# Kernel optimization log

Hardware: AMD Instinct MI355X
Metric: run time of the kernel (lower is better)

## Reference

```python
import jax, jax.numpy as jnp
import numpy as np
import math

MODEL_DIM = 256
NUM_HEADS = 8
HEAD_DIM = MODEL_DIM // NUM_HEADS
DEMAND_DIM = 3
H, W = 128, 256
N_COLLAB = 4


def conv1x1(x, w, b):
    # x: [B, Cin, H, W], w: [Cout, Cin], b: [Cout]
    return jnp.einsum('oi,bihw->bohw', w, x) + b[None, :, None, None]


def setup_inputs() -> dict:
    key = jax.random.key(0)
    ks = jax.random.split(key, 16)
    s = 0.02
    hid = MODEL_DIM // 2
    inp = {
        'ego_features': jax.random.normal(ks[0], (1, MODEL_DIM, H, W), jnp.float32),
        'ego_demand': jax.random.uniform(ks[1], (1, DEMAND_DIM, H, W), jnp.float32),
        'collaborator_features': jax.random.normal(ks[2], (N_COLLAB, MODEL_DIM, H, W), jnp.float32),
        'w_d1': jax.random.normal(ks[3], (hid, DEMAND_DIM), jnp.float32) * s,
        'b_d1': jnp.zeros((hid,), jnp.float32),
        'w_d2': jax.random.normal(ks[4], (MODEL_DIM, hid), jnp.float32) * s,
        'b_d2': jnp.zeros((MODEL_DIM,), jnp.float32),
        'wq': jax.random.normal(ks[5], (MODEL_DIM, MODEL_DIM), jnp.float32) * s,
        'bq': jnp.zeros((MODEL_DIM,), jnp.float32),
        'wk': jax.random.normal(ks[6], (MODEL_DIM, MODEL_DIM), jnp.float32) * s,
        'bk': jnp.zeros((MODEL_DIM,), jnp.float32),
        'wv': jax.random.normal(ks[7], (MODEL_DIM, MODEL_DIM), jnp.float32) * s,
        'bv': jnp.zeros((MODEL_DIM,), jnp.float32),
        'wo': jax.random.normal(ks[8], (MODEL_DIM, MODEL_DIM), jnp.float32) * s,
        'bo': jnp.zeros((MODEL_DIM,), jnp.float32),
        'pos_emb': jnp.zeros((1, MODEL_DIM, H, W), jnp.float32),
    }
    return inp


def reference(ego_features, ego_demand, collaborator_features,
              w_d1, b_d1, w_d2, b_d2, wq, bq, wk, bk, wv, bv, wo, bo, pos_emb):
    # demand encoder: 1x1 conv -> relu -> 1x1 conv
    enc = conv1x1(jax.nn.relu(conv1x1(ego_demand, w_d1, b_d1)), w_d2, b_d2)
    query_state = ego_features + enc + pos_emb  # [1, C, H, W]

    q = conv1x1(query_state, wq, bq).reshape(NUM_HEADS, HEAD_DIM, H, W)        # [M, d, H, W]
    k = conv1x1(collaborator_features, wk, bk).reshape(N_COLLAB, NUM_HEADS, HEAD_DIM, H, W)
    v = conv1x1(collaborator_features, wv, bv).reshape(N_COLLAB, NUM_HEADS, HEAD_DIM, H, W)

    scale = math.sqrt(HEAD_DIM)
    # per-pixel dot product over head_dim -> scores [N, M, H, W]
    scores = jnp.einsum('mdhw,nmdhw->nmhw', q, k) / scale
    attn = jax.nn.softmax(scores, axis=0)  # softmax over collaborators
    # weighted sum over collaborators -> [M, d, H, W]
    out = jnp.einsum('nmhw,nmdhw->mdhw', attn, v).reshape(1, MODEL_DIM, H, W)
    return conv1x1(out, wo, bo)  # [1, C, H, W]
```

## Files before the change

### kernel.cpp

```cpp
#include <hip/hip_runtime.h>
#include <stdint.h>

typedef __attribute__((ext_vector_type(8))) short short8;
typedef __attribute__((ext_vector_type(4))) float f32x4;

constexpr int C   = 256;
constexpr int HID = 128;
constexpr int P   = 32768;
constexpr int BN  = 64;
constexpr int XLD = 280;
constexpr int HLD = 136;

constexpr unsigned OFF_WQ  = 0;
constexpr unsigned OFF_WK  = 65536;
constexpr unsigned OFF_WV  = 131072;
constexpr unsigned OFF_WO  = 196608;
constexpr unsigned OFF_WD2 = 262144;
constexpr unsigned W_TOTAL = 294912;

__device__ __forceinline__ unsigned f2b(float x) {
    unsigned u = __float_as_uint(x);
    return (u + 0x7FFFu + ((u >> 16) & 1u)) >> 16;
}
__device__ __forceinline__ float b2f(unsigned u) {
    return __uint_as_float(u << 16);
}

__global__ void cvt_weights(const float* __restrict__ wq, const float* __restrict__ wk,
                            const float* __restrict__ wv, const float* __restrict__ wo,
                            const float* __restrict__ wd2, unsigned short* __restrict__ dst) {
    unsigned i = blockIdx.x * 256 + threadIdx.x;
    if (i >= W_TOTAL) return;
    float v;
    if (i < OFF_WK)       v = wq[i];
    else if (i < OFF_WV)  v = wk[i - OFF_WK];
    else if (i < OFF_WO)  v = wv[i - OFF_WV];
    else if (i < OFF_WD2) v = wo[i - OFF_WO];
    else                  v = wd2[i - OFF_WD2];
    dst[i] = (unsigned short)f2b(v);
}


template <int K, int LD, int MI, bool SWZ>
__device__ __forceinline__ void gemmW(const unsigned short* __restrict__ W,
                                      const unsigned short* __restrict__ B,
                                      int row0, int a, int q, f32x4 (*acc)[4]) {
#pragma unroll 2
    for (int ks = 0; ks < K / 32; ++ks) {
        const int kb = ks * 32 + q * 8;
        short8 af[MI], bf[4];
#pragma unroll
        for (int mi = 0; mi < MI; ++mi)
            af[mi] = *reinterpret_cast<const short8*>(W + (size_t)(row0 + mi * 16 + a) * K + kb);
#pragma unroll
        for (int ni = 0; ni < 4; ++ni) {
            const int col = SWZ ? (kb ^ (((2 * ni + (a >> 3)) & 7) << 3)) : kb;
            bf[ni] = *reinterpret_cast<const short8*>(B + (ni * 16 + a) * LD + col);
        }
#pragma unroll
        for (int mi = 0; mi < MI; ++mi)
#pragma unroll
            for (int ni = 0; ni < 4; ++ni)
                acc[mi][ni] = __builtin_amdgcn_mfma_f32_16x16x32_bf16(af[mi], bf[ni], acc[mi][ni], 0, 0, 0);
    }
}

__device__ __forceinline__ void stage_ego(const float* __restrict__ s0,
                                          const float* __restrict__ s1,
                                          int t, int pix0, unsigned short* X) {
    const int cg = t >> 4;
    const int pb = 4 * (t & 15);
    const int swz = (((t & 15) >> 1) & 7) << 3;
#pragma unroll
    for (int k = 0; k < 4; ++k) {
        const int c = 2 * cg + 64 * k;
        const int cs = c ^ swz;
        float4 ra = *reinterpret_cast<const float4*>(s0 + (size_t)c * P + pix0 + pb);
        float4 rb = *reinterpret_cast<const float4*>(s0 + (size_t)(c + 1) * P + pix0 + pb);
        float4 ta = *reinterpret_cast<const float4*>(s1 + (size_t)c * P + pix0 + pb);
        float4 tb = *reinterpret_cast<const float4*>(s1 + (size_t)(c + 1) * P + pix0 + pb);
        ra.x += ta.x; ra.y += ta.y; ra.z += ta.z; ra.w += ta.w;
        rb.x += tb.x; rb.y += tb.y; rb.z += tb.z; rb.w += tb.w;
        const float va[4] = {ra.x, ra.y, ra.z, ra.w};
        const float vb[4] = {rb.x, rb.y, rb.z, rb.w};
#pragma unroll
        for (int pi = 0; pi < 4; ++pi) {
            unsigned pk = f2b(va[pi]) | (f2b(vb[pi]) << 16);
            *reinterpret_cast<unsigned*>(X + (pb + pi) * XLD + cs) = pk;
        }
    }
}

__device__ __forceinline__ void issue_half(const float* __restrict__ src, int pix0,
                                           int t, int k0, float4* s4) {
    const int cg = t >> 4;
    const int pb = 4 * (t & 15);
#pragma unroll
    for (int kk = 0; kk < 2; ++kk) {
        const int c = 2 * cg + 64 * (k0 + kk);
        s4[2 * kk]     = *reinterpret_cast<const float4*>(src + (size_t)c * P + pix0 + pb);
        s4[2 * kk + 1] = *reinterpret_cast<const float4*>(src + (size_t)(c + 1) * P + pix0 + pb);
    }
}

__device__ __forceinline__ void convert_half(unsigned short* X, int t, int k0,
                                             const float4* s4) {
    const int cg = t >> 4;
    const int pb = 4 * (t & 15);
    const int swz = (((t & 15) >> 1) & 7) << 3;
#pragma unroll
    for (int kk = 0; kk < 2; ++kk) {
        const int cs = (2 * cg + 64 * (k0 + kk)) ^ swz;
        const float4 ra = s4[2 * kk], rb = s4[2 * kk + 1];
        const float va[4] = {ra.x, ra.y, ra.z, ra.w};
        const float vb[4] = {rb.x, rb.y, rb.z, rb.w};
#pragma unroll
        for (int pi = 0; pi < 4; ++pi) {
            unsigned pk = f2b(va[pi]) | (f2b(vb[pi]) << 16);
            *reinterpret_cast<unsigned*>(X + (pb + pi) * XLD + cs) = pk;
        }
    }
}

__global__ __launch_bounds__(512, 2) void dca_mfma(
    const float* __restrict__ ego, const float* __restrict__ dem,
    const float* __restrict__ col,
    const float* __restrict__ w_d1, const float* __restrict__ b_d1,
    const float* __restrict__ b_d2, const float* __restrict__ bq,
    const float* __restrict__ bk, const float* __restrict__ bv,
    const float* __restrict__ bo, const float* __restrict__ pos,
    const unsigned short* __restrict__ wbf, float* __restrict__ out)
{
    __shared__ __align__(16) unsigned short xbuf[2 * BN * XLD];
    unsigned short* const x0 = xbuf;
    unsigned short* const x1 = xbuf + BN * XLD;

    const int t = threadIdx.x;
    const int w = t >> 6;
    const int l = t & 63;
    const int a = l & 15;
    const int q = l >> 4;
    const int row0 = w * 32;
    const int pix0 = blockIdx.x * BN;

    stage_ego(ego, pos, t, pix0, x0);

    {
        const int hid0 = 2 * l;
        const float w10 = w_d1[hid0 * 3 + 0], w11 = w_d1[hid0 * 3 + 1], w12 = w_d1[hid0 * 3 + 2];
        const float w20 = w_d1[hid0 * 3 + 3], w21 = w_d1[hid0 * 3 + 4], w22 = w_d1[hid0 * 3 + 5];
        const float bb0 = b_d1[hid0], bb1 = b_d1[hid0 + 1];
#pragma unroll
        for (int k = 0; k < 8; ++k) {
            const int p = w + 8 * k;
            float d0 = dem[pix0 + p];
            float d1 = dem[P + pix0 + p];
            float d2v = dem[2 * P + pix0 + p];
            float h0 = fmaxf(bb0 + w10 * d0 + w11 * d1 + w12 * d2v, 0.0f);
            float h1v = fmaxf(bb1 + w20 * d0 + w21 * d1 + w22 * d2v, 0.0f);
            *reinterpret_cast<unsigned*>(x1 + p * HLD + hid0) = f2b(h0) | (f2b(h1v) << 16);
        }
    }
    __syncthreads();

    f32x4 vacc[2][4];

#pragma unroll
    for (int mi = 0; mi < 2; ++mi) {
        f32x4 bb = *reinterpret_cast<const f32x4*>(b_d2 + row0 + mi * 16 + q * 4);
#pragma unroll
        for (int ni = 0; ni < 4; ++ni) vacc[mi][ni] = bb;
    }
    gemmW<HID, HLD, 2, false>(wbf + OFF_WD2, x1, row0, a, q, vacc);
#pragma unroll
    for (int mi = 0; mi < 2; ++mi) {
        const int cb = row0 + mi * 16 + q * 4;
#pragma unroll
        for (int ni = 0; ni < 4; ++ni) {
            const int row = ni * 16 + a;
            const int cs = cb ^ (((2 * ni + (a >> 3)) & 7) << 3);
            unsigned* cell = reinterpret_cast<unsigned*>(x0 + row * XLD + cs);
            unsigned e0 = cell[0], e1 = cell[1];
            float o0 = vacc[mi][ni][0] + b2f(e0 & 0xFFFFu);
            float o1 = vacc[mi][ni][1] + b2f(e0 >> 16);
            float o2 = vacc[mi][ni][2] + b2f(e1 & 0xFFFFu);
            float o3 = vacc[mi][ni][3] + b2f(e1 >> 16);
            cell[0] = f2b(o0) | (f2b(o1) << 16);
            cell[1] = f2b(o2) | (f2b(o3) << 16);
        }
    }
    __syncthreads();

    float4 sA[4], sB[4];
    issue_half(col, pix0, t, 0, sA);

#pragma unroll
    for (int mi = 0; mi < 2; ++mi) {
        f32x4 bb = *reinterpret_cast<const f32x4*>(bq + row0 + mi * 16 + q * 4);
#pragma unroll
        for (int ni = 0; ni < 4; ++ni) vacc[mi][ni] = bb;
    }
    gemmW<C, XLD, 2, true>(wbf + OFF_WQ, x0, row0, a, q, vacc);
    unsigned qpk[2][4][2];
#pragma unroll
    for (int mi = 0; mi < 2; ++mi)
#pragma unroll
        for (int ni = 0; ni < 4; ++ni) {
            qpk[mi][ni][0] = f2b(vacc[mi][ni][0]) | (f2b(vacc[mi][ni][1]) << 16);
            qpk[mi][ni][1] = f2b(vacc[mi][ni][2]) | (f2b(vacc[mi][ni][3]) << 16);
        }

    convert_half(x1, t, 0, sA);
    issue_half(col, pix0, t, 2, sB);
    convert_half(x1, t, 2, sB);
    issue_half(col + (size_t)C * P, pix0, t, 0, sA);
    __syncthreads();

    float lrun[4];
#pragma unroll
    for (int ni = 0; ni < 4; ++ni) lrun[ni] = 0.0f;
    {
        const f32x4 z = {0.0f, 0.0f, 0.0f, 0.0f};
#pragma unroll
        for (int mi = 0; mi < 2; ++mi)
#pragma unroll
            for (int ni = 0; ni < 4; ++ni) vacc[mi][ni] = z;
    }
#pragma unroll 1
    for (int n = 0; n < 4; ++n) {
        unsigned short* const rbuf = (n & 1) ? x0 : x1;
        unsigned short* const wbuf = (n & 1) ? x1 : x0;
        float s[4];
#pragma unroll
        for (int ni = 0; ni < 4; ++ni) s[ni] = 0.0f;
        {
            f32x4 kacc[2][4];
#pragma unroll
            for (int mi = 0; mi < 2; ++mi) {
                f32x4 bb = *reinterpret_cast<const f32x4*>(bk + row0 + mi * 16 + q * 4);
#pragma unroll
                for (int ni = 0; ni < 4; ++ni) kacc[mi][ni] = bb;
            }
            gemmW<C, XLD, 2, true>(wbf + OFF_WK, rbuf, row0, a, q, kacc);
#pragma unroll
            for (int mi = 0; mi < 2; ++mi)
#pragma unroll
                for (int ni = 0; ni < 4; ++ni) {
                    const unsigned u0 = qpk[mi][ni][0], u1 = qpk[mi][ni][1];
                    float ps = s[ni];
                    ps += b2f(u0 & 0xFFFFu) * kacc[mi][ni][0];
                    ps += b2f(u0 >> 16)     * kacc[mi][ni][1];
                    ps += b2f(u1 & 0xFFFFu) * kacc[mi][ni][2];
                    ps += b2f(u1 >> 16)     * kacc[mi][ni][3];
                    s[ni] = ps;
                }
        }
        if (n < 3) {
            convert_half(wbuf, t, 0, sA);
            issue_half(col + (size_t)(n + 1) * C * P, pix0, t, 2, sB);
        }
        float pp[4];
#pragma unroll
        for (int ni = 0; ni < 4; ++ni) {
            float ps = s[ni];
            ps += __shfl_xor(ps, 16);
            ps += __shfl_xor(ps, 32);
            pp[ni] = __expf(ps * 0.17677669529663687f);
            lrun[ni] += pp[ni];
        }
#pragma unroll
        for (int ni = 0; ni < 4; ++ni) {
            const float ip = 1.0f / pp[ni];
#pragma unroll
            for (int mi = 0; mi < 2; ++mi) vacc[mi][ni] *= ip;
        }
        gemmW<C, XLD, 2, true>(wbf + OFF_WV, rbuf, row0, a, q, vacc);
#pragma unroll
        for (int ni = 0; ni < 4; ++ni) {
#pragma unroll
            for (int mi = 0; mi < 2; ++mi) vacc[mi][ni] *= pp[ni];
        }
        if (n < 3) convert_half(wbuf, t, 2, sB);
        if (n < 2) issue_half(col + (size_t)(n + 2) * C * P, pix0, t, 0, sA);
        __syncthreads();
    }
#pragma unroll
    for (int ni = 0; ni < 4; ++ni) {
        float inv = 1.0f / lrun[ni];
#pragma unroll
        for (int mi = 0; mi < 2; ++mi) vacc[mi][ni] *= inv;
    }
#pragma unroll
    for (int mi = 0; mi < 2; ++mi) {
        f32x4 bb = *reinterpret_cast<const f32x4*>(bv + row0 + mi * 16 + q * 4);
#pragma unroll
        for (int ni = 0; ni < 4; ++ni) vacc[mi][ni] += bb;
    }

#pragma unroll
    for (int mi = 0; mi < 2; ++mi) {
        const int cb = row0 + mi * 16 + q * 4;
#pragma unroll
        for (int ni = 0; ni < 4; ++ni) {
            const int row = ni * 16 + a;
            const int cs = cb ^ (((2 * ni + (a >> 3)) & 7) << 3);
            unsigned* cell = reinterpret_cast<unsigned*>(x0 + row * XLD + cs);
            cell[0] = f2b(vacc[mi][ni][0]) | (f2b(vacc[mi][ni][1]) << 16);
            cell[1] = f2b(vacc[mi][ni][2]) | (f2b(vacc[mi][ni][3]) << 16);
        }
    }
    __syncthreads();
#pragma unroll
    for (int mi = 0; mi < 2; ++mi) {
        f32x4 bb = *reinterpret_cast<const f32x4*>(bo + row0 + mi * 16 + q * 4);
#pragma unroll
        for (int ni = 0; ni < 4; ++ni) vacc[mi][ni] = bb;
    }
    gemmW<C, XLD, 2, true>(wbf + OFF_WO, x0, row0, a, q, vacc);
#pragma unroll
    for (int mi = 0; mi < 2; ++mi) {
        const int cb = row0 + mi * 16 + q * 4;
#pragma unroll
        for (int ni = 0; ni < 4; ++ni) {
            const int pix = pix0 + ni * 16 + a;
#pragma unroll
            for (int r = 0; r < 4; ++r)
                out[(size_t)(cb + r) * P + pix] = vacc[mi][ni][r];
        }
    }
}

extern "C" void kernel_launch(void* const* d_in, const int* in_sizes, int n_in,
                              void* d_out, int out_size, void* d_ws, size_t ws_size,
                              hipStream_t stream) {
    const float* ego  = (const float*)d_in[0];
    const float* dem  = (const float*)d_in[1];
    const float* col  = (const float*)d_in[2];
    const float* w_d1 = (const float*)d_in[3];
    const float* b_d1 = (const float*)d_in[4];
    const float* w_d2 = (const float*)d_in[5];
    const float* b_d2 = (const float*)d_in[6];
    const float* wq   = (const float*)d_in[7];
    const float* bq   = (const float*)d_in[8];
    const float* wk   = (const float*)d_in[9];
    const float* bk   = (const float*)d_in[10];
    const float* wv   = (const float*)d_in[11];
    const float* bv   = (const float*)d_in[12];
    const float* wo   = (const float*)d_in[13];
    const float* bo   = (const float*)d_in[14];
    const float* pos  = (const float*)d_in[15];
    float* out = (float*)d_out;
    unsigned short* wbf = (unsigned short*)d_ws;

    hipLaunchKernelGGL(cvt_weights, dim3((W_TOTAL + 255) / 256), dim3(256), 0, stream,
                       wq, wk, wv, wo, w_d2, wbf);
    hipLaunchKernelGGL(dca_mfma, dim3(P / BN), dim3(512), 0, stream,
                       ego, dem, col, w_d1, b_d1, b_d2, bq, bk, bv, bo, pos, wbf, out);
}
```

Baseline: 334.8 us.

## Use four LDS buffers to stage collaborator tiles with fewer barriers

Moves from two double-buffered LDS tiles to four, so all collaborator feature tiles are staged in whole-tile chunks (8 float4 loads per thread) instead of halves. This cuts the per-iteration __syncthreads, leaving one barrier mid-loop and one after it, and starts the first collaborator load earlier, before the demand GEMM. LDS use per block doubles to about 140KB, which likely cuts occupancy from two blocks per CU to one despite launch_bounds(512,2). Doubling the in-flight prefetch registers also adds register pressure.

```diff
diff --git a/kernel.cpp b/kernel.cpp
--- a/kernel.cpp
+++ b/kernel.cpp
@@ -91,27 +91,26 @@
     }
 }
 
-__device__ __forceinline__ void issue_half(const float* __restrict__ src, int pix0,
-                                           int t, int k0, float4* s4) {
+__device__ __forceinline__ void issue_tile(const float* __restrict__ src, int pix0,
+                                           int t, float4* s4) {
     const int cg = t >> 4;
     const int pb = 4 * (t & 15);
 #pragma unroll
-    for (int kk = 0; kk < 2; ++kk) {
-        const int c = 2 * cg + 64 * (k0 + kk);
-        s4[2 * kk]     = *reinterpret_cast<const float4*>(src + (size_t)c * P + pix0 + pb);
-        s4[2 * kk + 1] = *reinterpret_cast<const float4*>(src + (size_t)(c + 1) * P + pix0 + pb);
-    }
-}
-
-__device__ __forceinline__ void convert_half(unsigned short* X, int t, int k0,
-                                             const float4* s4) {
+    for (int k = 0; k < 4; ++k) {
+        const int c = 2 * cg + 64 * k;
+        s4[2 * k]     = *reinterpret_cast<const float4*>(src + (size_t)c * P + pix0 + pb);
+        s4[2 * k + 1] = *reinterpret_cast<const float4*>(src + (size_t)(c + 1) * P + pix0 + pb);
+    }
+}
+
+__device__ __forceinline__ void convert_tile(unsigned short* X, int t, const float4* s4) {
     const int cg = t >> 4;
     const int pb = 4 * (t & 15);
     const int swz = (((t & 15) >> 1) & 7) << 3;
 #pragma unroll
-    for (int kk = 0; kk < 2; ++kk) {
-        const int cs = (2 * cg + 64 * (k0 + kk)) ^ swz;
-        const float4 ra = s4[2 * kk], rb = s4[2 * kk + 1];
+    for (int k = 0; k < 4; ++k) {
+        const int cs = (2 * cg + 64 * k) ^ swz;
+        const float4 ra = s4[2 * k], rb = s4[2 * k + 1];
         const float va[4] = {ra.x, ra.y, ra.z, ra.w};
         const float vb[4] = {rb.x, rb.y, rb.z, rb.w};
 #pragma unroll
@@ -131,9 +130,11 @@
     const float* __restrict__ bo, const float* __restrict__ pos,
     const unsigned short* __restrict__ wbf, float* __restrict__ out)
 {
-    __shared__ __align__(16) unsigned short xbuf[2 * BN * XLD];
-    unsigned short* const x0 = xbuf;
-    unsigned short* const x1 = xbuf + BN * XLD;
+    __shared__ __align__(16) unsigned short xbuf[4 * BN * XLD];
+    unsigned short* const bufA = xbuf;
+    unsigned short* const bufB = xbuf + 1 * BN * XLD;
+    unsigned short* const bufC = xbuf + 2 * BN * XLD;
+    unsigned short* const bufD = xbuf + 3 * BN * XLD;
 
     const int t = threadIdx.x;
     const int w = t >> 6;
@@ -143,7 +144,7 @@
     const int row0 = w * 32;
     const int pix0 = blockIdx.x * BN;
 
-    stage_ego(ego, pos, t, pix0, x0);
+    stage_ego(ego, pos, t, pix0, bufA);
 
     {
         const int hid0 = 2 * l;
@@ -158,10 +159,13 @@
             float d2v = dem[2 * P + pix0 + p];
             float h0 = fmaxf(bb0 + w10 * d0 + w11 * d1 + w12 * d2v, 0.0f);
             float h1v = fmaxf(bb1 + w20 * d0 + w21 * d1 + w22 * d2v, 0.0f);
-            *reinterpret_cast<unsigned*>(x1 + p * HLD + hid0) = f2b(h0) | (f2b(h1v) << 16);
-        }
-    }
-    __syncthreads();
+            *reinterpret_cast<unsigned*>(bufD + p * HLD + hid0) = f2b(h0) | (f2b(h1v) << 16);
+        }
+    }
+    __syncthreads();
+
+    float4 sA[8];
+    issue_tile(col, pix0, t, sA);
 
     f32x4 vacc[2][4];
 
@@ -171,7 +175,7 @@
 #pragma unroll
         for (int ni = 0; ni < 4; ++ni) vacc[mi][ni] = bb;
     }
-    gemmW<HID, HLD, 2, false>(wbf + OFF_WD2, x1, row0, a, q, vacc);
+    gemmW<HID, HLD, 2, false>(wbf + OFF_WD2, bufD, row0, a, q, vacc);
 #pragma unroll
     for (int mi = 0; mi < 2; ++mi) {
         const int cb = row0 + mi * 16 + q * 4;
@@ -179,7 +183,7 @@
         for (int ni = 0; ni < 4; ++ni) {
             const int row = ni * 16 + a;
             const int cs = cb ^ (((2 * ni + (a >> 3)) & 7) << 3);
-            unsigned* cell = reinterpret_cast<unsigned*>(x0 + row * XLD + cs);
+            unsigned* cell = reinterpret_cast<unsigned*>(bufA + row * XLD + cs);
             unsigned e0 = cell[0], e1 = cell[1];
             float o0 = vacc[mi][ni][0] + b2f(e0 & 0xFFFFu);
             float o1 = vacc[mi][ni][1] + b2f(e0 >> 16);
@@ -191,8 +195,8 @@
     }
     __syncthreads();
 
-    float4 sA[4], sB[4];
-    issue_half(col, pix0, t, 0, sA);
+    convert_tile(bufB, t, sA);
+    issue_tile(col + (size_t)C * P, pix0, t, sA);
 
 #pragma unroll
     for (int mi = 0; mi < 2; ++mi) {
@@ -200,7 +204,7 @@
 #pragma unroll
         for (int ni = 0; ni < 4; ++ni) vacc[mi][ni] = bb;
     }
-    gemmW<C, XLD, 2, true>(wbf + OFF_WQ, x0, row0, a, q, vacc);
+    gemmW<C, XLD, 2, true>(wbf + OFF_WQ, bufA, row0, a, q, vacc);
     unsigned qpk[2][4][2];
 #pragma unroll
     for (int mi = 0; mi < 2; ++mi)
@@ -210,11 +214,10 @@
             qpk[mi][ni][1] = f2b(vacc[mi][ni][2]) | (f2b(vacc[mi][ni][3]) << 16);
         }
 
-    convert_half(x1, t, 0, sA);
-    issue_half(col, pix0, t, 2, sB);
-    convert_half(x1, t, 2, sB);
-    issue_half(col + (size_t)C * P, pix0, t, 0, sA);
-    __syncthreads();
+    convert_tile(bufC, t, sA);
+    __syncthreads();
+
+    issue_tile(col + (size_t)2 * C * P, pix0, t, sA);
 
     float lrun[4];
 #pragma unroll
@@ -228,8 +231,8 @@
     }
 #pragma unroll 1
     for (int n = 0; n < 4; ++n) {
-        unsigned short* const rbuf = (n & 1) ? x0 : x1;
-        unsigned short* const wbuf = (n & 1) ? x1 : x0;
+        if (n == 2) __syncthreads();
+        const unsigned short* rb = xbuf + (size_t)((n + 1) & 3) * (BN * XLD);
         float s[4];
 #pragma unroll
         for (int ni = 0; ni < 4; ++ni) s[ni] = 0.0f;
@@ -241,7 +244,7 @@
 #pragma unroll
                 for (int ni = 0; ni < 4; ++ni) kacc[mi][ni] = bb;
             }
-            gemmW<C, XLD, 2, true>(wbf + OFF_WK, rbuf, row0, a, q, kacc);
+            gemmW<C, XLD, 2, true>(wbf + OFF_WK, rb, row0, a, q, kacc);
 #pragma unroll
             for (int mi = 0; mi < 2; ++mi)
 #pragma unroll
@@ -255,10 +258,11 @@
                     s[ni] = ps;
                 }
         }
-        if (n < 3) {
-            convert_half(wbuf, t, 0, sA);
-            issue_half(col + (size_t)(n + 1) * C * P, pix0, t, 2, sB);
-        }
+        if (n == 0) {
+            convert_tile(bufD, t, sA);
+            issue_tile(col + (size_t)3 * C * P, pix0, t, sA);
+        }
+        if (n == 1) convert_tile(bufA, t, sA);
         float pp[4];
 #pragma unroll
         for (int ni = 0; ni < 4; ++ni) {
@@ -274,15 +278,12 @@
 #pragma unroll
             for (int mi = 0; mi < 2; ++mi) vacc[mi][ni] *= ip;
         }
-        gemmW<C, XLD, 2, true>(wbf + OFF_WV, rbuf, row0, a, q, vacc);
+        gemmW<C, XLD, 2, true>(wbf + OFF_WV, rb, row0, a, q, vacc);
 #pragma unroll
         for (int ni = 0; ni < 4; ++ni) {
 #pragma unroll
             for (int mi = 0; mi < 2; ++mi) vacc[mi][ni] *= pp[ni];
         }
-        if (n < 3) convert_half(wbuf, t, 2, sB);
-        if (n < 2) issue_half(col + (size_t)(n + 2) * C * P, pix0, t, 0, sA);
-        __syncthreads();
     }
 #pragma unroll
     for (int ni = 0; ni < 4; ++ni) {
@@ -297,6 +298,7 @@
         for (int ni = 0; ni < 4; ++ni) vacc[mi][ni] += bb;
     }
 
+    __syncthreads();
 #pragma unroll
     for (int mi = 0; mi < 2; ++mi) {
         const int cb = row0 + mi * 16 + q * 4;
@@ -304,7 +306,7 @@
         for (int ni = 0; ni < 4; ++ni) {
             const int row = ni * 16 + a;
             const int cs = cb ^ (((2 * ni + (a >> 3)) & 7) << 3);
-            unsigned* cell = reinterpret_cast<unsigned*>(x0 + row * XLD + cs);
+            unsigned* cell = reinterpret_cast<unsigned*>(bufB + row * XLD + cs);
             cell[0] = f2b(vacc[mi][ni][0]) | (f2b(vacc[mi][ni][1]) << 16);
             cell[1] = f2b(vacc[mi][ni][2]) | (f2b(vacc[mi][ni][3]) << 16);
         }
@@ -316,7 +318,7 @@
 #pragma unroll
         for (int ni = 0; ni < 4; ++ni) vacc[mi][ni] = bb;
     }
-    gemmW<C, XLD, 2, true>(wbf + OFF_WO, x0, row0, a, q, vacc);
+    gemmW<C, XLD, 2, true>(wbf + OFF_WO, bufB, row0, a, q, vacc);
 #pragma unroll
     for (int mi = 0; mi < 2; ++mi) {
         const int cb = row0 + mi * 16 + q * 4;
```

After: 343.7 us. 1.03x slower.
